# Kernel tuning notes

Measured on AMD Instinct MI355X. Metric: run time of the kernel, lower is better.

## Reference

```python
import jax, jax.numpy as jnp
import numpy as np

B, S, E, H, D, F = 2, 2048, 768, 12, 64, 3072
NEG_INF = float('-inf')


def _layernorm(x, g, b, eps=1e-5):
    mu = jnp.mean(x, axis=-1, keepdims=True)
    var = jnp.var(x, axis=-1, keepdims=True)
    return (x - mu) * jax.lax.rsqrt(var + eps) * g + b


def setup_inputs() -> dict:
    key = jax.random.key(0)
    ks = jax.random.split(key, 16)
    s = lambda fan_in: 1.0 / np.sqrt(fan_in)
    inp = {
        'x': jax.random.normal(ks[0], (B, S, E), jnp.float32),
        # per-head projections stacked: [H, E, D] (k uses q_proj in the source, so no Wk)
        'Wq': jax.random.normal(ks[1], (H, E, D), jnp.float32) * s(E),
        'bq': jnp.zeros((H, D), jnp.float32),
        'Wv': jax.random.normal(ks[2], (H, E, D), jnp.float32) * s(E),
        'bv': jnp.zeros((H, D), jnp.float32),
        'Wo': jax.random.normal(ks[3], (H * D, E), jnp.float32) * s(H * D),
        'bo': jnp.zeros((E,), jnp.float32),
        'ln1_g': jnp.ones((E,), jnp.float32),
        'ln1_b': jnp.zeros((E,), jnp.float32),
        'W1': jax.random.normal(ks[4], (E, F), jnp.float32) * s(E),
        'b1': jnp.zeros((F,), jnp.float32),
        'W2': jax.random.normal(ks[5], (F, F), jnp.float32) * s(F),
        'b2': jnp.zeros((F,), jnp.float32),
        'W3': jax.random.normal(ks[6], (F, E), jnp.float32) * s(F),
        'b3': jnp.zeros((E,), jnp.float32),
        'ln2_g': jnp.ones((E,), jnp.float32),
        'ln2_b': jnp.zeros((E,), jnp.float32),
        'input_mask': jax.random.randint(ks[7], (B, S), 0, 2, jnp.int32),
    }
    return inp


def _mha(x, input_mask, Wq, bq, Wv, bv, Wo, bo):
    # NOTE: source bug reproduced — keys computed with q_proj.
    q = jnp.einsum('bse,hed->bhsd', x, Wq) + bq[None, :, None, :]
    k = q  # k = self.q_proj(x)
    v = jnp.einsum('bse,hed->bhsd', x, Wv) + bv[None, :, None, :]
    scale = 1.0 / np.sqrt(D)
    scores = jnp.einsum('bhsd,bhtd->bhst', q, k) * scale  # [B,H,S,S]
    causal = jnp.tril(jnp.ones((S, S), bool))
    scores = jnp.where(causal[None, None], scores, NEG_INF)
    scores = jnp.where(input_mask[:, None, None, :] == 0, NEG_INF, scores)
    # rows that are all -inf get their diagonal entry set to 1 (source edge-case fix)
    row_bad = jnp.all(jnp.isneginf(scores), axis=-1)  # [B,H,S]
    eye = jnp.eye(S, dtype=bool)
    scores = jnp.where(row_bad[..., None] & eye[None, None], 1.0, scores)
    attn = jax.nn.softmax(scores, axis=-1)
    out = jnp.einsum('bhst,bhtd->bhsd', attn, v)  # [B,H,S,D]
    out = out.transpose(0, 2, 1, 3).reshape(B, S, H * D)  # concat heads
    return out @ Wo + bo


def _ff(x, W1, b1, W2, b2, W3, b3):
    h = jax.nn.relu(x @ W1 + b1)
    h = jax.nn.relu(h @ W2 + b2)
    return h @ W3 + b3


def reference(x, Wq, bq, Wv, bv, Wo, bo, ln1_g, ln1_b, W1, b1, W2, b2, W3, b3, ln2_g, ln2_b, input_mask):
    y = x + _mha(_layernorm(x, ln1_g, ln1_b), input_mask, Wq, bq, Wv, bv, Wo, bo)
    y = y + _ff(_layernorm(y, ln2_g, ln2_b), W1, b1, W2, b2, W3, b3)
    return y
```

## Files before the change

### kernel.cpp

```cpp
#include <hip/hip_runtime.h>
#include <hip/hip_bf16.h>
#include <math.h>

#define BB 2
#define SS 2048
#define EE 768
#define HH 12
#define DD 64
#define FF 3072
#define BSROWS (BB*SS)
#define HD (HH*DD)

typedef __hip_bfloat16 bf16;
typedef __attribute__((ext_vector_type(8))) short short8;
typedef __attribute__((ext_vector_type(4))) float f32x4;

__device__ inline void store_val(float* p, float v) { *p = v; }
__device__ inline void store_val(bf16* p, float v)  { *p = __float2bfloat16(v); }

__global__ __launch_bounds__(256)
void transpose_all(const float* __restrict__ Wq, const float* __restrict__ Wv,
                   const float* __restrict__ Wo, const float* __restrict__ W1,
                   const float* __restrict__ W2, const float* __restrict__ W3,
                   bf16* __restrict__ WqT, bf16* __restrict__ WvT,
                   bf16* __restrict__ WoT, bf16* __restrict__ W1T,
                   bf16* __restrict__ W2T, bf16* __restrict__ W3T)
{
    const int id = blockIdx.x;
    const float* in; bf16* out; int R, C, z = 0, local;
    if (id < 1152) {
        const bool isv = id >= 576;
        local = isv ? id - 576 : id;
        in = isv ? Wv : Wq; out = isv ? WvT : WqT;
        R = EE; C = DD;
        z = local / 48; local -= z * 48;
    } else if (id < 1728)  { in = Wo; out = WoT; R = HD; C = EE; local = id - 1152; }
    else if (id < 4032)    { in = W1; out = W1T; R = EE; C = FF; local = id - 1728; }
    else if (id < 13248)   { in = W2; out = W2T; R = FF; C = FF; local = id - 4032; }
    else                   { in = W3; out = W3T; R = FF; C = EE; local = id - 13248; }
    const int tiles_x = C >> 5;
    const int ty = local / tiles_x, tx = local - ty * tiles_x;
    const int r0 = ty * 32, c0 = tx * 32;
    const size_t zoff = (size_t)z * R * C;

    __shared__ float tile[32][33];
    const int t = threadIdx.x;
    const int lr = t >> 5, lc = t & 31;
    #pragma unroll
    for (int i = 0; i < 4; ++i)
        tile[lr + 8 * i][lc] = in[zoff + (size_t)(r0 + lr + 8 * i) * C + c0 + lc];
    __syncthreads();
    #pragma unroll
    for (int i = 0; i < 4; ++i)
        out[zoff + (size_t)(c0 + lr + 8 * i) * R + r0 + lc] =
            __float2bfloat16(tile[lc][lr + 8 * i]);
}

template<typename OutT>
__global__ __launch_bounds__(256)
void ln_kernel(const float* __restrict__ x, const float* __restrict__ g,
               const float* __restrict__ bt, OutT* __restrict__ o)
{
    const int row = blockIdx.x;
    const float* xr = x + (size_t)row * EE;
    const int t = threadIdx.x;
    float v0 = xr[t], v1 = xr[t + 256], v2 = xr[t + 512];
    float s = v0 + v1 + v2;
    #pragma unroll
    for (int off = 32; off > 0; off >>= 1) s += __shfl_xor(s, off);
    __shared__ float red[8];
    const int w = t >> 6;
    if ((t & 63) == 0) red[w] = s;
    __syncthreads();
    const float mean = (red[0] + red[1] + red[2] + red[3]) * (1.f / 768.f);
    float d0 = v0 - mean, d1 = v1 - mean, d2 = v2 - mean;
    float q = d0 * d0 + d1 * d1 + d2 * d2;
    #pragma unroll
    for (int off = 32; off > 0; off >>= 1) q += __shfl_xor(q, off);
    if ((t & 63) == 0) red[4 + w] = q;
    __syncthreads();
    const float var = (red[4] + red[5] + red[6] + red[7]) * (1.f / 768.f);
    const float rstd = rsqrtf(var + 1e-5f);
    OutT* orow = o + (size_t)row * EE;
    store_val(&orow[t],       d0 * rstd * g[t]       + bt[t]);
    store_val(&orow[t + 256], d1 * rstd * g[t + 256] + bt[t + 256]);
    store_val(&orow[t + 512], d2 * rstd * g[t + 512] + bt[t + 512]);
}

template<typename OutT, bool RELU, bool HAS_RES, bool VT = false>
__global__ __launch_bounds__(256, 2)
void mfma_gemm(const bf16* __restrict__ A, const bf16* __restrict__ Bt,
               const float* __restrict__ bias, const float* __restrict__ res,
               OutT* __restrict__ C, int M, int N, int K)
{
    __shared__ bf16 As[128 * 64];
    __shared__ bf16 Bs[128 * 64];
    const int t = threadIdx.x;
    const int lane = t & 63;
    const int w = t >> 6;
    const int wm = w >> 1, wn = w & 1;
    const int m0 = blockIdx.y * 128, n0 = blockIdx.x * 128;
    const int fr = lane & 15;
    const int fq = lane >> 4;

    f32x4 acc[4][4];
    #pragma unroll
    for (int i = 0; i < 4; ++i)
        #pragma unroll
        for (int j = 0; j < 4; ++j)
            acc[i][j] = (f32x4){0.f, 0.f, 0.f, 0.f};

    for (int k0 = 0; k0 < K; k0 += 64) {
        asm volatile("s_waitcnt lgkmcnt(0)" ::: "memory");
        __syncthreads();
        #pragma unroll
        for (int i = 0; i < 4; ++i) {
            const int p = (w * 4 + i) * 64 + lane;
            const int m = p >> 3;
            const int c = (p & 7) ^ (m & 7);
            const bf16* ga = &A [(size_t)(m0 + m) * K + k0 + c * 8];
            const bf16* gb = &Bt[(size_t)(n0 + m) * K + k0 + c * 8];
            bf16* la = &As[(size_t)(w * 4 + i) * 512];
            bf16* lb = &Bs[(size_t)(w * 4 + i) * 512];
            __builtin_amdgcn_global_load_lds(
                (const __attribute__((address_space(1))) unsigned int*)ga,
                (__attribute__((address_space(3))) unsigned int*)la, 16, 0, 0);
            __builtin_amdgcn_global_load_lds(
                (const __attribute__((address_space(1))) unsigned int*)gb,
                (__attribute__((address_space(3))) unsigned int*)lb, 16, 0, 0);
        }
        asm volatile("s_waitcnt vmcnt(0)" ::: "memory");
        __syncthreads();

        short8 af[4][2], bfr[4][2];
        #pragma unroll
        for (int mi = 0; mi < 4; ++mi) {
            const int row = wm * 64 + mi * 16 + fr;
            #pragma unroll
            for (int kh = 0; kh < 2; ++kh) {
                const int slot = (kh * 4 + fq) ^ (row & 7);
                af[mi][kh] = *(const short8*)&As[row * 64 + slot * 8];
            }
        }
        #pragma unroll
        for (int ni = 0; ni < 4; ++ni) {
            const int row = wn * 64 + ni * 16 + fr;
            #pragma unroll
            for (int kh = 0; kh < 2; ++kh) {
                const int slot = (kh * 4 + fq) ^ (row & 7);
                bfr[ni][kh] = *(const short8*)&Bs[row * 64 + slot * 8];
            }
        }
        #pragma unroll
        for (int mi = 0; mi < 4; ++mi)
            #pragma unroll
            for (int ni = 0; ni < 4; ++ni) {
                acc[mi][ni] = __builtin_amdgcn_mfma_f32_16x16x32_bf16(
                    af[mi][0], bfr[ni][0], acc[mi][ni], 0, 0, 0);
                acc[mi][ni] = __builtin_amdgcn_mfma_f32_16x16x32_bf16(
                    af[mi][1], bfr[ni][1], acc[mi][ni], 0, 0, 0);
            }
    }

    #pragma unroll
    for (int ni = 0; ni < 4; ++ni) {
        const int cn = n0 + wn * 64 + ni * 16 + fr;
        const float bv = bias[cn];
        #pragma unroll
        for (int mi = 0; mi < 4; ++mi) {
            const int rbase = m0 + wm * 64 + mi * 16 + fq * 4;
            if (VT) {
                const int bidx = rbase >> 11, sidx = rbase & (SS - 1);
                const int hh = cn >> 6, dd = cn & 63;
                alignas(8) bf16 tmp[4];
                #pragma unroll
                for (int j = 0; j < 4; ++j)
                    tmp[j] = __float2bfloat16(acc[mi][ni][j] + bv);
                *(ushort4*)((bf16*)C + (((size_t)(bidx * HH + hh) * 64 + dd) * SS + sidx))
                    = *(const ushort4*)tmp;
            } else {
                #pragma unroll
                for (int j = 0; j < 4; ++j) {
                    float v = acc[mi][ni][j] + bv;
                    if (HAS_RES) v += res[(size_t)(rbase + j) * N + cn];
                    if (RELU) v = fmaxf(v, 0.f);
                    store_val(&C[(size_t)(rbase + j) * N + cn], v);
                }
            }
        }
    }
}

__global__ __launch_bounds__(256, 2)
void mfma_gemm_qv(const bf16* __restrict__ A,
                  const bf16* __restrict__ Bq, const bf16* __restrict__ Bv,
                  const float* __restrict__ biasq, const float* __restrict__ biasv,
                  bf16* __restrict__ Cq, bf16* __restrict__ Cv)
{
    const int M = BSROWS, N = HD, K = EE;
    const bool isv = (blockIdx.z == 1);
    const bf16* Bt = isv ? Bv : Bq;
    const float* bias = isv ? biasv : biasq;

    __shared__ bf16 As[128 * 64];
    __shared__ bf16 Bs[128 * 64];
    const int t = threadIdx.x;
    const int lane = t & 63;
    const int w = t >> 6;
    const int wm = w >> 1, wn = w & 1;
    const int m0 = blockIdx.y * 128, n0 = blockIdx.x * 128;
    const int fr = lane & 15;
    const int fq = lane >> 4;

    f32x4 acc[4][4];
    #pragma unroll
    for (int i = 0; i < 4; ++i)
        #pragma unroll
        for (int j = 0; j < 4; ++j)
            acc[i][j] = (f32x4){0.f, 0.f, 0.f, 0.f};

    for (int k0 = 0; k0 < K; k0 += 64) {
        asm volatile("s_waitcnt lgkmcnt(0)" ::: "memory");
        __syncthreads();
        #pragma unroll
        for (int i = 0; i < 4; ++i) {
            const int p = (w * 4 + i) * 64 + lane;
            const int m = p >> 3;
            const int c = (p & 7) ^ (m & 7);
            const bf16* ga = &A [(size_t)(m0 + m) * K + k0 + c * 8];
            const bf16* gb = &Bt[(size_t)(n0 + m) * K + k0 + c * 8];
            bf16* la = &As[(size_t)(w * 4 + i) * 512];
            bf16* lb = &Bs[(size_t)(w * 4 + i) * 512];
            __builtin_amdgcn_global_load_lds(
                (const __attribute__((address_space(1))) unsigned int*)ga,
                (__attribute__((address_space(3))) unsigned int*)la, 16, 0, 0);
            __builtin_amdgcn_global_load_lds(
                (const __attribute__((address_space(1))) unsigned int*)gb,
                (__attribute__((address_space(3))) unsigned int*)lb, 16, 0, 0);
        }
        asm volatile("s_waitcnt vmcnt(0)" ::: "memory");
        __syncthreads();

        short8 af[4][2], bfr[4][2];
        #pragma unroll
        for (int mi = 0; mi < 4; ++mi) {
            const int row = wm * 64 + mi * 16 + fr;
            #pragma unroll
            for (int kh = 0; kh < 2; ++kh) {
                const int slot = (kh * 4 + fq) ^ (row & 7);
                af[mi][kh] = *(const short8*)&As[row * 64 + slot * 8];
            }
        }
        #pragma unroll
        for (int ni = 0; ni < 4; ++ni) {
            const int row = wn * 64 + ni * 16 + fr;
            #pragma unroll
            for (int kh = 0; kh < 2; ++kh) {
                const int slot = (kh * 4 + fq) ^ (row & 7);
                bfr[ni][kh] = *(const short8*)&Bs[row * 64 + slot * 8];
            }
        }
        #pragma unroll
        for (int mi = 0; mi < 4; ++mi)
            #pragma unroll
            for (int ni = 0; ni < 4; ++ni) {
                acc[mi][ni] = __builtin_amdgcn_mfma_f32_16x16x32_bf16(
                    af[mi][0], bfr[ni][0], acc[mi][ni], 0, 0, 0);
                acc[mi][ni] = __builtin_amdgcn_mfma_f32_16x16x32_bf16(
                    af[mi][1], bfr[ni][1], acc[mi][ni], 0, 0, 0);
            }
    }

    #pragma unroll
    for (int ni = 0; ni < 4; ++ni) {
        const int cn = n0 + wn * 64 + ni * 16 + fr;
        const float bv = bias[cn];
        #pragma unroll
        for (int mi = 0; mi < 4; ++mi) {
            const int rbase = m0 + wm * 64 + mi * 16 + fq * 4;
            if (isv) {
                const int bidx = rbase >> 11, sidx = rbase & (SS - 1);
                const int hh = cn >> 6, dd = cn & 63;
                alignas(8) bf16 tmp[4];
                #pragma unroll
                for (int j = 0; j < 4; ++j)
                    tmp[j] = __float2bfloat16(acc[mi][ni][j] + bv);
                *(ushort4*)(Cv + (((size_t)(bidx * HH + hh) * 64 + dd) * SS + sidx))
                    = *(const ushort4*)tmp;
            } else {
                #pragma unroll
                for (int j = 0; j < 4; ++j)
                    Cq[(size_t)(rbase + j) * N + cn]
                        = __float2bfloat16(acc[mi][ni][j] + bv);
            }
        }
    }
}

__global__ __launch_bounds__(256, 2)
void attn_mfma(const bf16* __restrict__ qg, const bf16* __restrict__ vtg,
               const int* __restrict__ maskg, bf16* __restrict__ outg)
{
    const int qt = (int)(gridDim.x - 1 - blockIdx.x);
    const int h  = blockIdx.y;
    const int b  = blockIdx.z;
    __shared__ bf16 Ks[64 * 64];
    __shared__ bf16 Vts[64 * 64];
    __shared__ bf16 Ps[64][72];
    const int t = threadIdx.x;
    const int lane = t & 63;
    const int w = t >> 6;
    const int fr = lane & 15;
    const int g  = lane >> 4;
    const int q0 = qt * 64;

    #pragma unroll
    for (int i = 0; i < 2; ++i) {
        const int pc = i * 256 + t;
        const int m = pc >> 3, c = (pc & 7) ^ (m & 7);
        const bf16* src = qg + ((size_t)(b * SS + q0 + m) * HD + h * 64 + c * 8);
        __builtin_amdgcn_global_load_lds(
            (const __attribute__((address_space(1))) unsigned int*)src,
            (__attribute__((address_space(3))) unsigned int*)&Ks[pc * 8], 16, 0, 0);
    }
    asm volatile("s_waitcnt vmcnt(0)" ::: "memory");
    __syncthreads();
    short8 qa[2];
    {
        const int row = w * 16 + fr;
        #pragma unroll
        for (int s = 0; s < 2; ++s) {
            const int slot = (s * 4 + g) ^ (row & 7);
            qa[s] = *(const short8*)&Ks[row * 64 + slot * 8];
        }
    }
    short8 ones;
    #pragma unroll
    for (int i = 0; i < 8; ++i) ones[i] = (short)0x3F80;

    f32x4 o_acc[4];
    #pragma unroll
    for (int i = 0; i < 4; ++i) o_acc[i] = (f32x4){0.f, 0.f, 0.f, 0.f};
    f32x4 acc_l = (f32x4){0.f, 0.f, 0.f, 0.f};
    float run_m[4];
    #pragma unroll
    for (int j = 0; j < 4; ++j) run_m[j] = -INFINITY;

    for (int kvt = 0; kvt <= qt; ++kvt) {
        const int kv0 = kvt * 64;
        asm volatile("s_waitcnt lgkmcnt(0)" ::: "memory");
        __syncthreads();
        #pragma unroll
        for (int i = 0; i < 2; ++i) {
            const int pc = i * 256 + t;
            const int m = pc >> 3, c = (pc & 7) ^ (m & 7);
            const bf16* ksrc = qg  + ((size_t)(b * SS + kv0 + m) * HD + h * 64 + c * 8);
            const bf16* vsrc = vtg + (((size_t)(b * HH + h) * 64 + m) * SS + kv0 + c * 8);
            __builtin_amdgcn_global_load_lds(
                (const __attribute__((address_space(1))) unsigned int*)ksrc,
                (__attribute__((address_space(3))) unsigned int*)&Ks[pc * 8], 16, 0, 0);
            __builtin_amdgcn_global_load_lds(
                (const __attribute__((address_space(1))) unsigned int*)vsrc,
                (__attribute__((address_space(3))) unsigned int*)&Vts[pc * 8], 16, 0, 0);
        }
        int mv[4];
        #pragma unroll
        for (int ni = 0; ni < 4; ++ni)
            mv[ni] = maskg[b * SS + kv0 + ni * 16 + fr];
        asm volatile("s_waitcnt vmcnt(0)" ::: "memory");
        __syncthreads();

        f32x4 acc_s[4];
        #pragma unroll
        for (int ni = 0; ni < 4; ++ni) acc_s[ni] = (f32x4){0.f, 0.f, 0.f, 0.f};
        __builtin_amdgcn_s_setprio(1);
        #pragma unroll
        for (int ni = 0; ni < 4; ++ni) {
            const int row = ni * 16 + fr;
            #pragma unroll
            for (int s = 0; s < 2; ++s) {
                const int slot = (s * 4 + g) ^ (row & 7);
                short8 kb = *(const short8*)&Ks[row * 64 + slot * 8];
                acc_s[ni] = __builtin_amdgcn_mfma_f32_16x16x32_bf16(
                    qa[s], kb, acc_s[ni], 0, 0, 0);
            }
        }
        __builtin_amdgcn_s_setprio(0);

        float sv[4][4], mj[4], alpha[4];
        #pragma unroll
        for (int j = 0; j < 4; ++j) mj[j] = -INFINITY;
        #pragma unroll
        for (int ni = 0; ni < 4; ++ni) {
            const int kvcol = kv0 + ni * 16 + fr;
            const bool mok = (mv[ni] != 0);
            #pragma unroll
            for (int j = 0; j < 4; ++j) {
                const int qrow = q0 + w * 16 + g * 4 + j;
                const bool valid = mok && (kvcol <= qrow);
                const float s = valid ? acc_s[ni][j] * 0.125f : -INFINITY;
                sv[ni][j] = s;
                mj[j] = fmaxf(mj[j], s);
            }
        }
        #pragma unroll
        for (int j = 0; j < 4; ++j) {
            #pragma unroll
            for (int off = 1; off < 16; off <<= 1)
                mj[j] = fmaxf(mj[j], __shfl_xor(mj[j], off));
            const float newm = fmaxf(run_m[j], mj[j]);
            const float al = (newm == -INFINITY) ? 1.f : __expf(run_m[j] - newm);
            #pragma unroll
            for (int ni = 0; ni < 4; ++ni) {
                float pv = (sv[ni][j] == -INFINITY) ? 0.f : __expf(sv[ni][j] - newm);
                if (kvt == qt && newm == -INFINITY) {
                    const int dloc = w * 16 + g * 4 + j;
                    if ((dloc >> 4) == ni && (dloc & 15) == fr) pv = 1.f;
                }
                sv[ni][j] = pv;
            }
            run_m[j] = newm;
            alpha[j] = al;
        }
        #pragma unroll
        for (int ni = 0; ni < 4; ++ni)
            #pragma unroll
            for (int j = 0; j < 4; ++j)
                Ps[w * 16 + g * 4 + j][ni * 16 + fr] = __float2bfloat16(sv[ni][j]);
        #pragma unroll
        for (int nt = 0; nt < 4; ++nt)
            #pragma unroll
            for (int j = 0; j < 4; ++j)
                o_acc[nt][j] *= alpha[j];
        #pragma unroll
        for (int j = 0; j < 4; ++j) acc_l[j] *= alpha[j];

        short8 pa[2];
        #pragma unroll
        for (int s = 0; s < 2; ++s)
            pa[s] = *(const short8*)&Ps[w * 16 + fr][s * 32 + g * 8];
        __builtin_amdgcn_s_setprio(1);
        #pragma unroll
        for (int nt = 0; nt < 4; ++nt) {
            const int row = nt * 16 + fr;
            #pragma unroll
            for (int s = 0; s < 2; ++s) {
                const int slot = (s * 4 + g) ^ (row & 7);
                short8 vb = *(const short8*)&Vts[row * 64 + slot * 8];
                o_acc[nt] = __builtin_amdgcn_mfma_f32_16x16x32_bf16(
                    pa[s], vb, o_acc[nt], 0, 0, 0);
            }
        }
        #pragma unroll
        for (int s = 0; s < 2; ++s)
            acc_l = __builtin_amdgcn_mfma_f32_16x16x32_bf16(
                pa[s], ones, acc_l, 0, 0, 0);
        __builtin_amdgcn_s_setprio(0);
    }

    float inv[4];
    #pragma unroll
    for (int j = 0; j < 4; ++j) inv[j] = (acc_l[j] > 0.f) ? 1.f / acc_l[j] : 0.f;
    #pragma unroll
    for (int nt = 0; nt < 4; ++nt)
        #pragma unroll
        for (int j = 0; j < 4; ++j)
            outg[(size_t)(b * SS + q0 + w * 16 + g * 4 + j) * HD + h * 64 + nt * 16 + fr]
                = __float2bfloat16(o_acc[nt][j] * inv[j]);
}

extern "C" void kernel_launch(void* const* d_in, const int* in_sizes, int n_in,
                              void* d_out, int out_size, void* d_ws, size_t ws_size,
                              hipStream_t stream)
{
    const float* x    = (const float*)d_in[0];
    const float* Wq   = (const float*)d_in[1];
    const float* bq   = (const float*)d_in[2];
    const float* Wv   = (const float*)d_in[3];
    const float* bv   = (const float*)d_in[4];
    const float* Wo   = (const float*)d_in[5];
    const float* bo   = (const float*)d_in[6];
    const float* ln1g = (const float*)d_in[7];
    const float* ln1b = (const float*)d_in[8];
    const float* W1   = (const float*)d_in[9];
    const float* b1   = (const float*)d_in[10];
    const float* W2   = (const float*)d_in[11];
    const float* b2   = (const float*)d_in[12];
    const float* W3   = (const float*)d_in[13];
    const float* b3   = (const float*)d_in[14];
    const float* ln2g = (const float*)d_in[15];
    const float* ln2b = (const float*)d_in[16];
    const int*   mask = (const int*)d_in[17];
    float* out = (float*)d_out;
    char* wsb  = (char*)d_ws;

    size_t off = 0;
    bf16* WqT = (bf16*)(wsb + off); off += (size_t)EE * HD * 2;
    bf16* WvT = (bf16*)(wsb + off); off += (size_t)EE * HD * 2;
    bf16* WoT = (bf16*)(wsb + off); off += (size_t)HD * EE * 2;
    bf16* W1T = (bf16*)(wsb + off); off += (size_t)EE * FF * 2;
    bf16* W3T = (bf16*)(wsb + off); off += (size_t)FF * EE * 2;
    bf16* W2T = (bf16*)(wsb + off); off += (size_t)FF * FF * 2;
    bf16* qbf = (bf16*)(wsb + off);
    bf16* h1  = qbf;                  off += (size_t)BSROWS * HD * 2;
    bf16* vt  = (bf16*)(wsb + off);   off += (size_t)BSROWS * HD * 2;
    bf16* attno = (bf16*)(wsb + off); off += (size_t)BSROWS * HD * 2;
                 off += (size_t)BSROWS * HD * 2;
    bf16* xln = (bf16*)(wsb + off);   off += (size_t)BSROWS * EE * 2;
    bf16* h2  = (bf16*)(wsb + off);   off += (size_t)BSROWS * FF * 2;
    float* y1 = (float*)(wsb + off);  off += (size_t)BSROWS * EE * 4;

    transpose_all<<<15552, 256, 0, stream>>>(Wq, Wv, Wo, W1, W2, W3,
                                             WqT, WvT, WoT, W1T, W2T, W3T);
    ln_kernel<bf16><<<BSROWS, 256, 0, stream>>>(x, ln1g, ln1b, xln);
    dim3 gp(HD / 128, BSROWS / 128);
    mfma_gemm_qv<<<dim3(gp.x, gp.y, 2), 256, 0, stream>>>(
        xln, WqT, WvT, bq, bv, qbf, vt);
    attn_mfma<<<dim3(SS/64, HH, BB), 256, 0, stream>>>(qbf, vt, mask, attno);
    mfma_gemm<float, false, true><<<gp, 256, 0, stream>>>(attno, WoT, bo, x, y1, BSROWS, EE, HD);
    bf16* y1ln = xln;
    ln_kernel<bf16><<<BSROWS, 256, 0, stream>>>(y1, ln2g, ln2b, y1ln);
    dim3 gf(FF / 128, BSROWS / 128);
    mfma_gemm<bf16, true, false><<<gf, 256, 0, stream>>>(y1ln, W1T, b1, nullptr, h1, BSROWS, FF, EE);
    mfma_gemm<bf16, true, false><<<gf, 256, 0, stream>>>(h1, W2T, b2, nullptr, h2, BSROWS, FF, FF);
    mfma_gemm<float, false, true><<<gp, 256, 0, stream>>>(h2, W3T, b3, y1, out, BSROWS, EE, FF);
}
```

Measured before the change: 313.8 us.

## Add 256x256 double-buffered MFMA GEMM for the FFN W1 and W2 layers

Adds a new GEMM kernel with 256x256 output tiles, 512 threads, and double-buffered LDS filled by direct global-to-LDS loads with an XOR swizzle. It is used for the two large feed-forward GEMMs (W1, W2) in place of the 128x128 kernel. Bigger tiles raise operand reuse per LDS load, and prefetching the next K tile overlaps memory with MFMA work. The catch is 128 KB of LDS and 128 accumulator registers per thread, so only one block fits per CU, and the grid has just 192 blocks for 256 CUs.

New measurement: 333.5 us. +6.3%, slower.

```diff
diff --git a/kernel.cpp b/kernel.cpp
--- a/kernel.cpp
+++ b/kernel.cpp
@@ -191,6 +191,117 @@
     }
 }
 
+template<typename OutT, bool RELU>
+__global__ __launch_bounds__(512, 1)
+void gemm256(const bf16* __restrict__ A, const bf16* __restrict__ Bt,
+             const float* __restrict__ bias, OutT* __restrict__ C,
+             int M, int N, int K)
+{
+    __shared__ bf16 As[2][256 * 64];
+    __shared__ bf16 Bs[2][256 * 64];
+    const int t = threadIdx.x;
+    const int lane = t & 63;
+    const int w = t >> 6;
+    const int wm = w >> 2, wn = w & 3;
+    const int m0 = blockIdx.y * 256, n0 = blockIdx.x * 256;
+    const int fr = lane & 15;
+    const int fq = lane >> 4;
+    const int NT = K >> 6;
+
+#define STAGE_G(T, BUF) do {                                                   \
+        const int k0_ = (T) << 6;                                              \
+        _Pragma("unroll")                                                      \
+        for (int i_ = 0; i_ < 4; ++i_) {                                       \
+            const int p_ = i_ * 512 + t;                    \
+            const int m_ = p_ >> 3, c_ = (p_ & 7) ^ (m_ & 7);                  \
+            const bf16* ga_ = &A [(size_t)(m0 + m_) * K + k0_ + c_ * 8];       \
+            const bf16* gb_ = &Bt[(size_t)(n0 + m_) * K + k0_ + c_ * 8];       \
+            __builtin_amdgcn_global_load_lds(                                  \
+                (const __attribute__((address_space(1))) unsigned int*)ga_,    \
+                (__attribute__((address_space(3))) unsigned int*)&As[BUF][p_ * 8], \
+                16, 0, 0);                                                     \
+            __builtin_amdgcn_global_load_lds(                                  \
+                (const __attribute__((address_space(1))) unsigned int*)gb_,    \
+                (__attribute__((address_space(3))) unsigned int*)&Bs[BUF][p_ * 8], \
+                16, 0, 0);                                                     \
+        }                                                                      \
+    } while (0)
+
+    f32x4 acc[8][4];
+    #pragma unroll
+    for (int i = 0; i < 8; ++i)
+        #pragma unroll
+        for (int j = 0; j < 4; ++j)
+            acc[i][j] = (f32x4){0.f, 0.f, 0.f, 0.f};
+
+    STAGE_G(0, 0);
+    asm volatile("s_waitcnt vmcnt(0)" ::: "memory");
+    __builtin_amdgcn_s_barrier();
+    asm volatile("" ::: "memory");
+
+    for (int T = 0; T < NT; ++T) {
+        const int db = T & 1;
+        if (T + 1 < NT) STAGE_G(T + 1, db ^ 1);
+
+        short8 bfr[4][2];
+        #pragma unroll
+        for (int ni = 0; ni < 4; ++ni) {
+            const int row = wn * 64 + ni * 16 + fr;
+            #pragma unroll
+            for (int s = 0; s < 2; ++s) {
+                const int slot = (s * 4 + fq) ^ (row & 7);
+                bfr[ni][s] = *(const short8*)&Bs[db][row * 64 + slot * 8];
+            }
+        }
+        #pragma unroll
+        for (int mq = 0; mq < 2; ++mq) {
+            short8 af[4][2];
+            #pragma unroll
+            for (int mi = 0; mi < 4; ++mi) {
+                const int row = wm * 128 + mq * 64 + mi * 16 + fr;
+                #pragma unroll
+                for (int s = 0; s < 2; ++s) {
+                    const int slot = (s * 4 + fq) ^ (row & 7);
+                    af[mi][s] = *(const short8*)&As[db][row * 64 + slot * 8];
+                }
+            }
+            __builtin_amdgcn_s_setprio(1);
+            #pragma unroll
+            for (int mi = 0; mi < 4; ++mi)
+                #pragma unroll
+                for (int ni = 0; ni < 4; ++ni) {
+                    acc[mq * 4 + mi][ni] = __builtin_amdgcn_mfma_f32_16x16x32_bf16(
+                        af[mi][0], bfr[ni][0], acc[mq * 4 + mi][ni], 0, 0, 0);
+                    acc[mq * 4 + mi][ni] = __builtin_amdgcn_mfma_f32_16x16x32_bf16(
+                        af[mi][1], bfr[ni][1], acc[mq * 4 + mi][ni], 0, 0, 0);
+                }
+            __builtin_amdgcn_s_setprio(0);
+        }
+
+        asm volatile("s_waitcnt lgkmcnt(0)" ::: "memory");
+        if (T + 1 < NT) asm volatile("s_waitcnt vmcnt(0)" ::: "memory");
+        __builtin_amdgcn_s_barrier();
+        asm volatile("" ::: "memory");
+    }
+#undef STAGE_G
+
+    #pragma unroll
+    for (int ni = 0; ni < 4; ++ni) {
+        const int cn = n0 + wn * 64 + ni * 16 + fr;
+        const float bv = bias[cn];
+        #pragma unroll
+        for (int mi = 0; mi < 8; ++mi) {
+            const int rbase = m0 + wm * 128 + mi * 16 + fq * 4;
+            #pragma unroll
+            for (int j = 0; j < 4; ++j) {
+                float v = acc[mi][ni][j] + bv;
+                if (RELU) v = fmaxf(v, 0.f);
+                store_val(&C[(size_t)(rbase + j) * N + cn], v);
+            }
+        }
+    }
+}
+
 __global__ __launch_bounds__(256, 2)
 void mfma_gemm_qv(const bf16* __restrict__ A,
                   const bf16* __restrict__ Bq, const bf16* __restrict__ Bv,
@@ -520,8 +631,8 @@
     mfma_gemm<float, false, true><<<gp, 256, 0, stream>>>(attno, WoT, bo, x, y1, BSROWS, EE, HD);
     bf16* y1ln = xln;
     ln_kernel<bf16><<<BSROWS, 256, 0, stream>>>(y1, ln2g, ln2b, y1ln);
-    dim3 gf(FF / 128, BSROWS / 128);
-    mfma_gemm<bf16, true, false><<<gf, 256, 0, stream>>>(y1ln, W1T, b1, nullptr, h1, BSROWS, FF, EE);
-    mfma_gemm<bf16, true, false><<<gf, 256, 0, stream>>>(h1, W2T, b2, nullptr, h2, BSROWS, FF, FF);
+    dim3 g256(FF / 256, BSROWS / 256);
+    gemm256<bf16, true><<<g256, 512, 0, stream>>>(y1ln, W1T, b1, h1, BSROWS, FF, EE);
+    gemm256<bf16, true><<<g256, 512, 0, stream>>>(h1, W2T, b2, h2, BSROWS, FF, FF);
     mfma_gemm<float, false, true><<<gp, 256, 0, stream>>>(h2, W3T, b3, y1, out, BSROWS, EE, FF);
 }
```

## Use 256x256 eight-phase pipelined MFMA GEMM for the W1 and W2 FFN layers

Applied to the files above, without the earlier changes.

Adds a 512-thread GEMM kernel with 256x256 tiles and double-buffered LDS, filled through direct global-to-LDS loads with an XOR swizzle. Each 64-wide K tile is split into four compute phases, and each phase issues part of the next tile's loads alongside its MFMAs, using setprio and explicit waitcnt control. The W1 and W2 GEMMs switch from 128x128 tiles to this kernel to get more operand reuse and better load/compute overlap. In exchange, the grid has only 192 blocks at one block per CU, which may underfill a 256-CU device.

After: 342.9 us. 1.09x slower.

```diff
diff --git a/kernel.cpp b/kernel.cpp
--- a/kernel.cpp
+++ b/kernel.cpp
@@ -191,6 +191,146 @@
     }
 }
 
+template<typename OutT, bool RELU>
+__global__ __launch_bounds__(512, 1)
+void gemm256_8ph(const bf16* __restrict__ A, const bf16* __restrict__ Bt,
+                 const float* __restrict__ bias, OutT* __restrict__ C,
+                 int M, int N, int K)
+{
+    __shared__ bf16 As[2][256 * 64];
+    __shared__ bf16 Bs[2][256 * 64];
+    const int t = threadIdx.x;
+    const int lane = t & 63;
+    const int w = t >> 6;
+    const int wm = w >> 2, wn = w & 3;
+    const int m0 = blockIdx.y * 256, n0 = blockIdx.x * 256;
+    const int fr = lane & 15;
+    const int fq = lane >> 4;
+    const int NT = K >> 6;
+
+#define STAGE_A8(T, U) do {                                                    \
+        const int k0_ = (T) * 64;                                              \
+        _Pragma("unroll")                                                      \
+        for (int i_ = 0; i_ < 2; ++i_) {                                       \
+            const int p_ = i_ * 512 + t;                                       \
+            const int rl_ = p_ >> 3;                                           \
+            const int row_ = ((rl_ >> 6) << 7) + (U) * 64 + (rl_ & 63);        \
+            const int c_ = (p_ & 7) ^ (row_ & 7);                              \
+            const bf16* g_ = &A[(size_t)(m0 + row_) * K + k0_ + c_ * 8];       \
+            __builtin_amdgcn_global_load_lds(                                  \
+                (const __attribute__((address_space(1))) unsigned int*)g_,     \
+                (__attribute__((address_space(3))) unsigned int*)              \
+                    &As[(T) & 1][row_ * 64 + (p_ & 7) * 8], 16, 0, 0);         \
+        }                                                                      \
+    } while (0)
+
+#define STAGE_B8(T, V) do {                                                    \
+        const int k0_ = (T) * 64;                                              \
+        _Pragma("unroll")                                                      \
+        for (int i_ = 0; i_ < 2; ++i_) {                                       \
+            const int p_ = i_ * 512 + t;                                       \
+            const int rl_ = p_ >> 3;                                           \
+            const int row_ = (V) * 32 + ((rl_ >> 5) << 6) + (rl_ & 31);        \
+            const int c_ = (p_ & 7) ^ (row_ & 7);                              \
+            const bf16* g_ = &Bt[(size_t)(n0 + row_) * K + k0_ + c_ * 8];      \
+            __builtin_amdgcn_global_load_lds(                                  \
+                (const __attribute__((address_space(1))) unsigned int*)g_,     \
+                (__attribute__((address_space(3))) unsigned int*)              \
+                    &Bs[(T) & 1][row_ * 64 + (p_ & 7) * 8], 16, 0, 0);         \
+        }                                                                      \
+    } while (0)
+
+#define PHASE8(DB, MH, NH, STAGE_STMT, VM_STMT) do {                           \
+        short8 af_[4][2], bf_[2][2];                                           \
+        _Pragma("unroll")                                                      \
+        for (int m2 = 0; m2 < 4; ++m2) {                                       \
+            const int row = wm * 128 + (MH) * 64 + m2 * 16 + fr;               \
+            _Pragma("unroll")                                                  \
+            for (int ks = 0; ks < 2; ++ks) {                                   \
+                const int slot = (ks * 4 + fq) ^ (row & 7);                    \
+                af_[m2][ks] = *(const short8*)&As[DB][row * 64 + slot * 8];    \
+            }                                                                  \
+        }                                                                      \
+        _Pragma("unroll")                                                      \
+        for (int n2 = 0; n2 < 2; ++n2) {                                       \
+            const int row = wn * 64 + (NH) * 32 + n2 * 16 + fr;                \
+            _Pragma("unroll")                                                  \
+            for (int ks = 0; ks < 2; ++ks) {                                   \
+                const int slot = (ks * 4 + fq) ^ (row & 7);                    \
+                bf_[n2][ks] = *(const short8*)&Bs[DB][row * 64 + slot * 8];    \
+            }                                                                  \
+        }                                                                      \
+        STAGE_STMT;                                                            \
+        __builtin_amdgcn_s_barrier();                                          \
+        asm volatile("s_waitcnt lgkmcnt(0)" ::: "memory");                     \
+        __builtin_amdgcn_sched_barrier(0);                                     \
+        __builtin_amdgcn_s_setprio(1);                                         \
+        _Pragma("unroll")                                                      \
+        for (int m2 = 0; m2 < 4; ++m2)                                         \
+            _Pragma("unroll")                                                  \
+            for (int n2 = 0; n2 < 2; ++n2) {                                   \
+                acc[(MH) * 4 + m2][(NH) * 2 + n2] =                            \
+                    __builtin_amdgcn_mfma_f32_16x16x32_bf16(                   \
+                        af_[m2][0], bf_[n2][0],                                \
+                        acc[(MH) * 4 + m2][(NH) * 2 + n2], 0, 0, 0);           \
+                acc[(MH) * 4 + m2][(NH) * 2 + n2] =                            \
+                    __builtin_amdgcn_mfma_f32_16x16x32_bf16(                   \
+                        af_[m2][1], bf_[n2][1],                                \
+                        acc[(MH) * 4 + m2][(NH) * 2 + n2], 0, 0, 0);           \
+            }                                                                  \
+        __builtin_amdgcn_s_setprio(0);                                         \
+        VM_STMT;                                                               \
+        __builtin_amdgcn_s_barrier();                                          \
+    } while (0)
+
+    f32x4 acc[8][4];
+    #pragma unroll
+    for (int i = 0; i < 8; ++i)
+        #pragma unroll
+        for (int j = 0; j < 4; ++j)
+            acc[i][j] = (f32x4){0.f, 0.f, 0.f, 0.f};
+
+    STAGE_A8(0, 0); STAGE_A8(0, 1); STAGE_B8(0, 0); STAGE_B8(0, 1);
+    STAGE_A8(1, 0); STAGE_B8(1, 0);
+    asm volatile("s_waitcnt vmcnt(4)" ::: "memory");
+    __builtin_amdgcn_s_barrier();
+
+    for (int it = 0; it < (NT >> 1); ++it) {
+        const int T0 = 2 * it;
+        const bool more = (T0 + 2 < NT);
+        PHASE8(0, 0, 0, STAGE_A8(T0 + 1, 1), (void)0);
+        PHASE8(0, 0, 1, STAGE_B8(T0 + 1, 1), (void)0);
+        PHASE8(0, 1, 0, if (more) STAGE_A8(T0 + 2, 0), (void)0);
+        PHASE8(0, 1, 1, if (more) STAGE_B8(T0 + 2, 0),
+               if (more) { asm volatile("s_waitcnt vmcnt(4)" ::: "memory"); }
+               else      { asm volatile("s_waitcnt vmcnt(0)" ::: "memory"); });
+        PHASE8(1, 0, 0, if (more) STAGE_A8(T0 + 2, 1), (void)0);
+        PHASE8(1, 0, 1, if (more) STAGE_B8(T0 + 2, 1), (void)0);
+        PHASE8(1, 1, 0, if (more) STAGE_A8(T0 + 3, 0), (void)0);
+        PHASE8(1, 1, 1, if (more) STAGE_B8(T0 + 3, 0),
+               if (more) { asm volatile("s_waitcnt vmcnt(4)" ::: "memory"); });
+    }
+#undef PHASE8
+#undef STAGE_A8
+#undef STAGE_B8
+
+    #pragma unroll
+    for (int ni = 0; ni < 4; ++ni) {
+        const int cn = n0 + wn * 64 + ni * 16 + fr;
+        const float bv = bias[cn];
+        #pragma unroll
+        for (int mi = 0; mi < 8; ++mi) {
+            const int rbase = m0 + wm * 128 + mi * 16 + fq * 4;
+            #pragma unroll
+            for (int j = 0; j < 4; ++j) {
+                float v = acc[mi][ni][j] + bv;
+                if (RELU) v = fmaxf(v, 0.f);
+                store_val(&C[(size_t)(rbase + j) * N + cn], v);
+            }
+        }
+    }
+}
+
 __global__ __launch_bounds__(256, 2)
 void mfma_gemm_qv(const bf16* __restrict__ A,
                   const bf16* __restrict__ Bq, const bf16* __restrict__ Bv,
@@ -520,8 +660,8 @@
     mfma_gemm<float, false, true><<<gp, 256, 0, stream>>>(attno, WoT, bo, x, y1, BSROWS, EE, HD);
     bf16* y1ln = xln;
     ln_kernel<bf16><<<BSROWS, 256, 0, stream>>>(y1, ln2g, ln2b, y1ln);
-    dim3 gf(FF / 128, BSROWS / 128);
-    mfma_gemm<bf16, true, false><<<gf, 256, 0, stream>>>(y1ln, W1T, b1, nullptr, h1, BSROWS, FF, EE);
-    mfma_gemm<bf16, true, false><<<gf, 256, 0, stream>>>(h1, W2T, b2, nullptr, h2, BSROWS, FF, FF);
+    dim3 g256(FF / 256, BSROWS / 256);
+    gemm256_8ph<bf16, true><<<g256, 512, 0, stream>>>(y1ln, W1T, b1, h1, BSROWS, FF, EE);
+    gemm256_8ph<bf16, true><<<g256, 512, 0, stream>>>(h1, W2T, b2, h2, BSROWS, FF, FF);
     mfma_gemm<float, false, true><<<gp, 256, 0, stream>>>(h2, W3T, b3, y1, out, BSROWS, EE, FF);
 }
```
